# Optimization experiments

Measured on AMD Instinct MI355X. Metric: run time of the kernel, lower is better.

## Reference

```python
import jax, jax.numpy as jnp
import numpy as np

B, F, Q, CHUNK = 2, 8192, 4096, 512
NUM_VERTS = 6000


def _safe_div(n, d):
    return n / jnp.where(d == 0, 1.0, d)


def _bary(a, b, c, p):
    """Barycentric coords of the closest point on triangle (a,b,c) to p.
    All args broadcastable [..., 3]; returns [..., 3] (u, v, w) with
    closest = u*a + v*b + w*c. Ericson, Real-Time Collision Detection."""
    ab = b - a; ac = c - a; ap = p - a
    d1 = jnp.sum(ab * ap, -1); d2 = jnp.sum(ac * ap, -1)
    bp = p - b
    d3 = jnp.sum(ab * bp, -1); d4 = jnp.sum(ac * bp, -1)
    cp_ = p - c
    d5 = jnp.sum(ab * cp_, -1); d6 = jnp.sum(ac * cp_, -1)
    vc = d1 * d4 - d3 * d2
    vb = d5 * d2 - d1 * d6
    va = d3 * d6 - d5 * d4
    v_ab = _safe_div(d1, d1 - d3)
    w_ac = _safe_div(d2, d2 - d6)
    w_bc = _safe_div(d4 - d3, (d4 - d3) + (d5 - d6))
    inv = _safe_div(1.0, va + vb + vc)
    v_in = vb * inv; w_in = vc * inv
    zero = jnp.zeros_like(d1); one = jnp.ones_like(d1)
    conds = [(d1 <= 0) & (d2 <= 0),
             (d3 >= 0) & (d4 <= d3),
             (vc <= 0) & (d1 >= 0) & (d3 <= 0),
             (d6 >= 0) & (d5 <= d6),
             (vb <= 0) & (d2 >= 0) & (d6 <= 0),
             (va <= 0) & (d4 >= d3) & (d5 >= d6)]
    u = jnp.select(conds, [one, zero, 1 - v_ab, zero, 1 - w_ac, zero], 1 - v_in - w_in)
    v = jnp.select(conds, [zero, one, v_ab, zero, zero, 1 - w_bc], v_in)
    w = jnp.select(conds, [zero, zero, zero, one, w_ac, w_bc], w_in)
    return jnp.stack([u, v, w], -1)


def _closest_faces(triangles, points, chunk=CHUNK):
    """Exact closest-triangle index per query point (replaces BVH search).
    triangles [B,F,3,3], points [B,Q,3] -> int32 [B,Q]."""
    tri = jax.lax.stop_gradient(triangles)
    pts = jax.lax.stop_gradient(points)
    bsz, nq = pts.shape[0], pts.shape[1]
    a = tri[:, :, 0]; b = tri[:, :, 1]; c = tri[:, :, 2]  # [B,F,3]

    def one_chunk(p_chunk):  # [B,CH,3]
        pa = p_chunk[:, :, None, :]                       # [B,CH,1,3]
        bc = _bary(a[:, None], b[:, None], c[:, None], pa)  # [B,CH,F,3]
        cp = (bc[..., 0:1] * a[:, None] + bc[..., 1:2] * b[:, None]
              + bc[..., 2:3] * c[:, None])                # [B,CH,F,3]
        d2 = jnp.sum((cp - pa) ** 2, -1)                  # [B,CH,F]
        return jnp.argmin(d2, axis=-1)                    # [B,CH]

    chunks = jnp.moveaxis(pts.reshape(bsz, nq // chunk, chunk, 3), 1, 0)
    idx = jax.lax.map(one_chunk, chunks)                  # [NC,B,CH]
    return jnp.moveaxis(idx, 0, 1).reshape(bsz, nq)


def setup_inputs() -> dict:
    key = jax.random.key(0)
    k1, k2, k3, k4, k5 = jax.random.split(key, 5)
    return {
        'triangles': jax.random.normal(k1, (B, F, 3, 3), dtype=jnp.float32),
        'points': jax.random.normal(k2, (B, Q, 3), dtype=jnp.float32),
        'normals': jax.random.normal(k3, (B, F, 3, 3), dtype=jnp.float32),
        'cmaps': jax.random.normal(k4, (B, F, 3, 3), dtype=jnp.float32),
        'faces': jax.random.randint(k5, (B, F, 3), 0, NUM_VERTS, dtype=jnp.int32),
    }


def reference(triangles, points, normals, cmaps, faces):
    closest_faces = _closest_faces(triangles, points)     # [B,Q]
    idx = closest_faces[:, :, None, None]
    tri_g = jnp.take_along_axis(triangles, idx, axis=1)   # [B,Q,3,3]
    nrm_g = jnp.take_along_axis(normals, idx, axis=1)
    cmp_g = jnp.take_along_axis(cmaps, idx, axis=1)
    bcs = _bary(tri_g[:, :, 0], tri_g[:, :, 1], tri_g[:, :, 2], points)  # [B,Q,3]
    bcs = jnp.clip(bcs, 0.0, 1.0)
    closest_points = jnp.einsum('bqk,bqkd->bqd', bcs, tri_g)
    closest_normals = jnp.einsum('bqk,bqkd->bqd', bcs, nrm_g)
    closest_cmaps = jnp.einsum('bqk,bqkd->bqd', bcs, cmp_g)
    residual = closest_points - points
    closest_fids = jnp.take_along_axis(faces, closest_faces[:, :, None], axis=1)  # [B,Q,3]
    closest_idx = jnp.take_along_axis(
        closest_fids, jnp.argmax(bcs, -1)[:, :, None], axis=2)[..., 0]            # [B,Q]
    return residual, closest_normals, closest_cmaps, closest_idx
```

## Files before the change

kernel.cpp:

```cpp
#include <hip/hip_runtime.h>
#include <float.h>

#define B_   2
#define F_   8192
#define Q_   4096
#define NC   128
#define FC   (F_/NC)
#define PTS  256
#define PPT  4

typedef float f4u __attribute__((ext_vector_type(4), aligned(4)));
typedef unsigned int uint;

__device__ __forceinline__ float clamp01s(float x) {
    return fminf(fmaxf(x, 0.f), 1.f);
}

__device__ __forceinline__ void bary_uvw(
    float ax, float ay, float az,
    float bx, float by, float bz,
    float cx, float cy, float cz,
    float px, float py, float pz,
    float& u, float& v, float& w)
{
#pragma clang fp contract(off)
    float abx = bx - ax, aby = by - ay, abz = bz - az;
    float acx = cx - ax, acy = cy - ay, acz = cz - az;
    float apx = px - ax, apy = py - ay, apz = pz - az;
    float d1 = abx*apx + aby*apy + abz*apz;
    float d2 = acx*apx + acy*apy + acz*apz;
    float bpx = px - bx, bpy = py - by, bpz = pz - bz;
    float d3 = abx*bpx + aby*bpy + abz*bpz;
    float d4 = acx*bpx + acy*bpy + acz*bpz;
    float qx = px - cx, qy = py - cy, qz = pz - cz;
    float d5 = abx*qx + aby*qy + abz*qz;
    float d6 = acx*qx + acy*qy + acz*qz;
    float vc = d1*d4 - d3*d2;
    float vb = d5*d2 - d1*d6;
    float va = d3*d6 - d5*d4;

    bool c1 = (d1 <= 0.f) && (d2 <= 0.f);
    bool c2 = (d3 >= 0.f) && (d4 <= d3);
    bool c3 = (vc <= 0.f) && (d1 >= 0.f) && (d3 <= 0.f);
    bool c4 = (d6 >= 0.f) && (d5 <= d6);
    bool c5 = (vb <= 0.f) && (d2 >= 0.f) && (d6 <= 0.f);
    bool c6 = (va <= 0.f) && (d4 >= d3) && (d5 >= d6);

    bool e1 = c1;
    bool p1 = !c1;
    bool e2 = p1 && c2;
    bool p2 = p1 && !c2;
    bool e3 = p2 && c3;
    bool p3 = p2 && !c3;
    bool e4 = p3 && c4;
    bool p4 = p3 && !c4;
    bool e5 = p4 && c5;
    bool p5 = p4 && !c5;
    bool e6 = p5 && c6;

    float d43 = d4 - d3;
    float d56 = d5 - d6;
    float n  = e3 ? d1        : (e5 ? d2        : (e6 ? d43         : 1.f));
    float dd = e3 ? (d1 - d3) : (e5 ? (d2 - d6) : (e6 ? (d43 + d56) : (va + vb + vc)));
    dd = (dd == 0.f) ? 1.f : dd;
    float t = n / dd;

    float vi = vb * t;
    float wi = vc * t;
    u = e1 ? 1.f : (e2 ? 0.f : (e3 ? 1.f - t : (e4 ? 0.f : (e5 ? 1.f - t : (e6 ? 0.f     : 1.f - vi - wi)))));
    v = e1 ? 0.f : (e2 ? 1.f : (e3 ? t       : (e4 ? 0.f : (e5 ? 0.f     : (e6 ? 1.f - t : vi)))));
    w = e1 ? 0.f : (e2 ? 0.f : (e3 ? 0.f     : (e4 ? 1.f : (e5 ? t       : (e6 ? t       : wi)))));
}

__global__ __launch_bounds__(PTS, 4) void scan_kernel(
    const float* __restrict__ tri, const float* __restrict__ pts,
    uint2* __restrict__ keys)
{
    constexpr int IM = ~(FC - 1);
    __shared__ float4 SC[FC * 5];
    __shared__ float4 SR[FC * 3];
    const int tid = threadIdx.x;
    const int pb = blockIdx.x, cb = blockIdx.y, bb = blockIdx.z;

    if (tid < FC) {
        const float* g = tri + ((size_t)bb * F_ + (size_t)cb * FC + tid) * 9;
        float ax = g[0], ay = g[1], az = g[2];
        float bx = g[3], by = g[4], bz = g[5];
        float cx = g[6], cy = g[7], cz = g[8];
        float abx = bx - ax, aby = by - ay, abz = bz - az;
        float acx = cx - ax, acy = cy - ay, acz = cz - az;
        float daa = abx*abx + aby*aby + abz*abz;
        float dcc = acx*acx + acy*acy + acz*acz;
        float dac = abx*acx + aby*acy + abz*acz;
        float dbc = daa + dcc - 2.f*dac;
        float nn  = daa*dcc - dac*dac;
        SC[tid*5 + 0] = make_float4(abx, aby, abz, -(abx*ax + aby*ay + abz*az));
        SC[tid*5 + 1] = make_float4(acx, acy, acz, -(acx*ax + acy*ay + acz*az));
        SC[tid*5 + 2] = make_float4(-2.f*ax, -2.f*ay, -2.f*az, ax*ax + ay*ay + az*az);
        SC[tid*5 + 3] = make_float4(daa, dcc, dac, nn);
        SC[tid*5 + 4] = make_float4(1.f/daa, 1.f/dcc, 1.f/dbc, 1.f/nn);
        SR[tid*3 + 0] = make_float4(ax, ay, az, 0.f);
        SR[tid*3 + 1] = make_float4(bx, by, bz, 0.f);
        SR[tid*3 + 2] = make_float4(cx, cy, cz, 0.f);
    }
    __syncthreads();

    const int q0 = pb * (PTS * PPT) + tid * PPT;
    const float* p0 = pts + ((size_t)bb * Q_ + q0) * 3;
    f4u l0 = *(const f4u*)(p0);
    f4u l1 = *(const f4u*)(p0 + 4);
    f4u l2 = *(const f4u*)(p0 + 8);
    float pxs[4] = {l0.x, l0.w, l1.z, l2.y};
    float pys[4] = {l0.y, l1.x, l1.w, l2.z};
    float pzs[4] = {l0.z, l1.y, l2.x, l2.w};
    float pps[4];
    #pragma unroll
    for (int p = 0; p < 4; ++p)
        pps[p] = pxs[p]*pxs[p] + pys[p]*pys[p] + pzs[p]*pzs[p];

    int K0[4] = {0x7FFFFFFF, 0x7FFFFFFF, 0x7FFFFFFF, 0x7FFFFFFF};
    int K1[4] = {0x7FFFFFFF, 0x7FFFFFFF, 0x7FFFFFFF, 0x7FFFFFFF};

    #pragma unroll 2
    for (int fl = 0; fl < FC; ++fl) {
        float4 c0 = SC[fl*5 + 0];
        float4 c1 = SC[fl*5 + 1];
        float4 c2 = SC[fl*5 + 2];
        float4 c3 = SC[fl*5 + 3];
        float4 c4 = SC[fl*5 + 4];
        float daa = c3.x, dcc = c3.y, dac = c3.z, nn = c3.w;
        float kk  = daa - dac;
        float dbc = daa + dcc - 2.f*dac;

        #pragma unroll
        for (int p = 0; p < 4; ++p) {
            float px = pxs[p], py = pys[p], pz = pzs[p];
            float d1 = fmaf(c0.x, px, fmaf(c0.y, py, fmaf(c0.z, pz, c0.w)));
            float d2 = fmaf(c1.x, px, fmaf(c1.y, py, fmaf(c1.z, pz, c1.w)));
            float s  = fmaf(c2.x, px, fmaf(c2.y, py, fmaf(c2.z, pz, c2.w)));
            float app = s + pps[p];

            float t1 = d1*dcc - d2*dac;
            float t2 = d2*daa - d1*dac;
            float ts = t1 + t2;
            float t12n = nn - ts;
            float ins  = fminf(fminf(t1, t2), t12n);
            float sgr  = (d1*t1 + d2*t2) * c4.w;

            float td1 = d1 + d1;
            float tab = clamp01s(d1 * c4.x);
            float rab = tab * (td1 - tab*daa);
            float td2 = d2 + d2;
            float tac = clamp01s(d2 * c4.y);
            float rac = tac * (td2 - tac*dcc);
            float d43 = (d2 - d1) + kk;
            float sbc = clamp01s(d43 * c4.z);
            float rbc = (td1 - daa) + sbc * ((d43 + d43) - sbc*dbc);
            float rmax = fmaxf(fmaxf(rab, rac), rbc);

            float red = (ins >= 0.f) ? sgr : rmax;
            float d = app - red;

            int k = (__float_as_int(d) & IM) | fl;
            int m = max(K0[p], k);
            K0[p] = min(K0[p], k);
            K1[p] = min(K1[p], m);
        }
    }

    #pragma unroll
    for (int p = 0; p < 4; ++p) {
        float px = pxs[p], py = pys[p], pz = pzs[p];
        float dbest = FLT_MAX; int fbest = 0x7FFFFFFF;
        #pragma unroll
        for (int j = 0; j < 2; ++j) {
            int lf = (j == 0 ? K0[p] : K1[p]) & (FC - 1);
            float4 ra = SR[lf*3 + 0];
            float4 rb = SR[lf*3 + 1];
            float4 rc = SR[lf*3 + 2];
            float u, v, w;
            bary_uvw(ra.x, ra.y, ra.z, rb.x, rb.y, rb.z, rc.x, rc.y, rc.z,
                     px, py, pz, u, v, w);
            float d2v;
            {
#pragma clang fp contract(off)
                float cpx = u*ra.x + v*rb.x + w*rc.x;
                float cpy = u*ra.y + v*rb.y + w*rc.y;
                float cpz = u*ra.z + v*rb.z + w*rc.z;
                float dx = cpx - px, dy = cpy - py, dz = cpz - pz;
                d2v = dx*dx + dy*dy + dz*dz;
            }
            int face = cb * FC + lf;
            if (d2v < dbest || (d2v == dbest && face < fbest)) { dbest = d2v; fbest = face; }
        }
        keys[((size_t)bb * Q_ + q0 + p) * NC + cb] = make_uint2(__float_as_uint(dbest), (uint)fbest);
    }
}

__global__ __launch_bounds__(256) void finalize_kernel(
    const float* __restrict__ tri, const float* __restrict__ pts,
    const float* __restrict__ nrm, const float* __restrict__ cmp,
    const int* __restrict__ faces,
    const uint2* __restrict__ keys,
    float* __restrict__ out)
{
#pragma clang fp contract(off)
    const int lane = threadIdx.x & 63;
    const int t = blockIdx.x * 4 + (threadIdx.x >> 6);
    const int bb = t >> 12;

    uint4 K = ((const uint4*)keys)[(size_t)t * (NC/2) + lane];
    float dbest = __uint_as_float(K.x); int fbest = (int)K.y;
    float d1v   = __uint_as_float(K.z); int f1v   = (int)K.w;
    if (d1v < dbest || (d1v == dbest && f1v < fbest)) { dbest = d1v; fbest = f1v; }
    for (int off = 32; off > 0; off >>= 1) {
        float od = __shfl_down(dbest, off);
        int   of = __shfl_down(fbest, off);
        if (od < dbest || (od == dbest && of < fbest)) { dbest = od; fbest = of; }
    }
    if (lane != 0) return;

    const float* pp = pts + (size_t)t * 3;
    float px = pp[0], py = pp[1], pz = pp[2];

    const int bestf = fbest;
    const float* tg = tri + ((size_t)bb * F_ + bestf) * 9;
    const float* ng = nrm + ((size_t)bb * F_ + bestf) * 9;
    const float* cg = cmp + ((size_t)bb * F_ + bestf) * 9;
    f4u TA = *(const f4u*)(tg), TB = *(const f4u*)(tg + 4);
    float TC = tg[8];
    f4u NA = *(const f4u*)(ng), NB = *(const f4u*)(ng + 4);
    float NCs = ng[8];
    f4u CA = *(const f4u*)(cg), CB = *(const f4u*)(cg + 4);
    float CC = cg[8];

    float u, v, w;
    bary_uvw(TA.x, TA.y, TA.z, TA.w, TB.x, TB.y, TB.z, TB.w, TC,
             px, py, pz, u, v, w);
    u = fminf(fmaxf(u, 0.f), 1.f);
    v = fminf(fmaxf(v, 0.f), 1.f);
    w = fminf(fmaxf(w, 0.f), 1.f);

    float cpx = u * TA.x + v * TA.w + w * TB.z;
    float cpy = u * TA.y + v * TB.x + w * TB.w;
    float cpz = u * TA.z + v * TB.y + w * TC;
    float nx  = u * NA.x + v * NA.w + w * NB.z;
    float ny  = u * NA.y + v * NB.x + w * NB.w;
    float nz  = u * NA.z + v * NB.y + w * NCs;
    float mx  = u * CA.x + v * CA.w + w * CB.z;
    float my  = u * CA.y + v * CB.x + w * CB.w;
    float mz  = u * CA.z + v * CB.y + w * CC;

    const size_t S3 = (size_t)B_ * Q_ * 3;
    out[(size_t)t * 3 + 0] = cpx - px;
    out[(size_t)t * 3 + 1] = cpy - py;
    out[(size_t)t * 3 + 2] = cpz - pz;
    out[S3 + (size_t)t * 3 + 0] = nx;
    out[S3 + (size_t)t * 3 + 1] = ny;
    out[S3 + (size_t)t * 3 + 2] = nz;
    out[2 * S3 + (size_t)t * 3 + 0] = mx;
    out[2 * S3 + (size_t)t * 3 + 1] = my;
    out[2 * S3 + (size_t)t * 3 + 2] = mz;

    int k = 0; float mm = u;
    if (v > mm) { mm = v; k = 1; }
    if (w > mm) { k = 2; }
    out[3 * S3 + t] = (float)faces[((size_t)bb * F_ + bestf) * 3 + k];
}

extern "C" void kernel_launch(void* const* d_in, const int* in_sizes, int n_in,
                              void* d_out, int out_size, void* d_ws, size_t ws_size,
                              hipStream_t stream) {
    const float* tri   = (const float*)d_in[0];
    const float* pts   = (const float*)d_in[1];
    const float* nrm   = (const float*)d_in[2];
    const float* cmp   = (const float*)d_in[3];
    const int*   faces = (const int*)d_in[4];
    float* out = (float*)d_out;

    uint2* keys = (uint2*)d_ws;

    dim3 g1(Q_ / (PTS * PPT), NC, B_);
    scan_kernel<<<g1, PTS, 0, stream>>>(tri, pts, keys);
    finalize_kernel<<<(B_ * Q_) / 4, 256, 0, stream>>>(
        tri, pts, nrm, cmp, faces, keys, out);
}
```

Baseline: 146.3 us.

## Precompute triangle constants in separate kernel and read them from global memory

Moves the per-triangle constant setup out of the scan kernel into a new precompute kernel that writes six float4s per face to workspace. The scan kernel then drops its shared-memory staging and barrier and reads the constants straight from global memory, which are uniform across the block and so likely become scalar loads. Points per thread drop from four to two and the occupancy hint rises from 4 to 8. This trades one extra launch and fewer points per constant fetch for no LDS use and higher occupancy.

```diff
diff --git a/kernel.cpp b/kernel.cpp
--- a/kernel.cpp
+++ b/kernel.cpp
@@ -7,9 +7,10 @@
 #define NC   128
 #define FC   (F_/NC)
 #define PTS  256
-#define PPT  4
+#define PPT  2
 
 typedef float f4u __attribute__((ext_vector_type(4), aligned(4)));
+typedef float f2u __attribute__((ext_vector_type(2), aligned(8)));
 typedef unsigned int uint;
 
 __device__ __forceinline__ float clamp01s(float x) {
@@ -72,121 +73,145 @@
     w = e1 ? 0.f : (e2 ? 0.f : (e3 ? 0.f     : (e4 ? 1.f : (e5 ? t       : (e6 ? t       : wi)))));
 }
 
-__global__ __launch_bounds__(PTS, 4) void scan_kernel(
+__global__ void precompute_kernel(const float* __restrict__ tri,
+                                  float4* __restrict__ cons)
+{
+    int i = blockIdx.x * blockDim.x + threadIdx.x;
+    if (i >= B_ * F_) return;
+    const float* g = tri + (size_t)i * 9;
+    float ax = g[0], ay = g[1], az = g[2];
+    float bx = g[3], by = g[4], bz = g[5];
+    float cx = g[6], cy = g[7], cz = g[8];
+    float abx = bx - ax, aby = by - ay, abz = bz - az;
+    float acx = cx - ax, acy = cy - ay, acz = cz - az;
+    float daa = abx*abx + aby*aby + abz*abz;
+    float dcc = acx*acx + acy*acy + acz*acz;
+    float dac = abx*acx + aby*acy + abz*acz;
+    float dbc = daa + dcc - 2.f*dac;
+    float nn  = daa*dcc - dac*dac;
+    float4* o = cons + (size_t)i * 6;
+    o[0] = make_float4(abx, aby, abz, -(abx*ax + aby*ay + abz*az));
+    o[1] = make_float4(acx, acy, acz, -(acx*ax + acy*ay + acz*az));
+    o[2] = make_float4(-2.f*ax, -2.f*ay, -2.f*az, ax*ax + ay*ay + az*az);
+    o[3] = make_float4(daa, dcc, -dac, nn);
+    o[4] = make_float4(1.f/daa, 1.f/dcc, 1.f/dbc, 1.f/nn);
+    o[5] = make_float4(daa - dac, dbc, 0.f, 0.f);
+}
+
+__global__ __launch_bounds__(PTS, 8) void scan_kernel(
     const float* __restrict__ tri, const float* __restrict__ pts,
-    uint2* __restrict__ keys)
+    const float4* __restrict__ cons, uint2* __restrict__ keys)
 {
     constexpr int IM = ~(FC - 1);
-    __shared__ float4 SC[FC * 5];
-    __shared__ float4 SR[FC * 3];
     const int tid = threadIdx.x;
     const int pb = blockIdx.x, cb = blockIdx.y, bb = blockIdx.z;
 
-    if (tid < FC) {
-        const float* g = tri + ((size_t)bb * F_ + (size_t)cb * FC + tid) * 9;
-        float ax = g[0], ay = g[1], az = g[2];
-        float bx = g[3], by = g[4], bz = g[5];
-        float cx = g[6], cy = g[7], cz = g[8];
-        float abx = bx - ax, aby = by - ay, abz = bz - az;
-        float acx = cx - ax, acy = cy - ay, acz = cz - az;
-        float daa = abx*abx + aby*aby + abz*abz;
-        float dcc = acx*acx + acy*acy + acz*acz;
-        float dac = abx*acx + aby*acy + abz*acz;
-        float dbc = daa + dcc - 2.f*dac;
-        float nn  = daa*dcc - dac*dac;
-        SC[tid*5 + 0] = make_float4(abx, aby, abz, -(abx*ax + aby*ay + abz*az));
-        SC[tid*5 + 1] = make_float4(acx, acy, acz, -(acx*ax + acy*ay + acz*az));
-        SC[tid*5 + 2] = make_float4(-2.f*ax, -2.f*ay, -2.f*az, ax*ax + ay*ay + az*az);
-        SC[tid*5 + 3] = make_float4(daa, dcc, dac, nn);
-        SC[tid*5 + 4] = make_float4(1.f/daa, 1.f/dcc, 1.f/dbc, 1.f/nn);
-        SR[tid*3 + 0] = make_float4(ax, ay, az, 0.f);
-        SR[tid*3 + 1] = make_float4(bx, by, bz, 0.f);
-        SR[tid*3 + 2] = make_float4(cx, cy, cz, 0.f);
-    }
-    __syncthreads();
-
     const int q0 = pb * (PTS * PPT) + tid * PPT;
     const float* p0 = pts + ((size_t)bb * Q_ + q0) * 3;
-    f4u l0 = *(const f4u*)(p0);
-    f4u l1 = *(const f4u*)(p0 + 4);
-    f4u l2 = *(const f4u*)(p0 + 8);
-    float pxs[4] = {l0.x, l0.w, l1.z, l2.y};
-    float pys[4] = {l0.y, l1.x, l1.w, l2.z};
-    float pzs[4] = {l0.z, l1.y, l2.x, l2.w};
-    float pps[4];
-    #pragma unroll
-    for (int p = 0; p < 4; ++p)
-        pps[p] = pxs[p]*pxs[p] + pys[p]*pys[p] + pzs[p]*pzs[p];
-
-    int K0[4] = {0x7FFFFFFF, 0x7FFFFFFF, 0x7FFFFFFF, 0x7FFFFFFF};
-    int K1[4] = {0x7FFFFFFF, 0x7FFFFFFF, 0x7FFFFFFF, 0x7FFFFFFF};
+    f2u m0 = *(const f2u*)(p0);
+    f2u m1 = *(const f2u*)(p0 + 2);
+    f2u m2 = *(const f2u*)(p0 + 4);
+    float px0 = m0.x, py0 = m0.y, pz0 = m1.x;
+    float px1 = m1.y, py1 = m2.x, pz1 = m2.y;
+    float pp0 = px0*px0 + py0*py0 + pz0*pz0;
+    float pp1 = px1*px1 + py1*py1 + pz1*pz1;
+
+    const float4* ct = cons + ((size_t)bb * F_ + (size_t)cb * FC) * 6;
+
+    int K00 = 0x7FFFFFFF, K01 = 0x7FFFFFFF;
+    int K10 = 0x7FFFFFFF, K11 = 0x7FFFFFFF;
 
     #pragma unroll 2
     for (int fl = 0; fl < FC; ++fl) {
-        float4 c0 = SC[fl*5 + 0];
-        float4 c1 = SC[fl*5 + 1];
-        float4 c2 = SC[fl*5 + 2];
-        float4 c3 = SC[fl*5 + 3];
-        float4 c4 = SC[fl*5 + 4];
-        float daa = c3.x, dcc = c3.y, dac = c3.z, nn = c3.w;
-        float kk  = daa - dac;
-        float dbc = daa + dcc - 2.f*dac;
-
-        #pragma unroll
-        for (int p = 0; p < 4; ++p) {
-            float px = pxs[p], py = pys[p], pz = pzs[p];
-            float d1 = fmaf(c0.x, px, fmaf(c0.y, py, fmaf(c0.z, pz, c0.w)));
-            float d2 = fmaf(c1.x, px, fmaf(c1.y, py, fmaf(c1.z, pz, c1.w)));
-            float s  = fmaf(c2.x, px, fmaf(c2.y, py, fmaf(c2.z, pz, c2.w)));
-            float app = s + pps[p];
-
-            float t1 = d1*dcc - d2*dac;
-            float t2 = d2*daa - d1*dac;
-            float ts = t1 + t2;
-            float t12n = nn - ts;
+        float4 T0 = ct[fl*6 + 0];
+        float4 T1 = ct[fl*6 + 1];
+        float4 T2 = ct[fl*6 + 2];
+        float4 T3 = ct[fl*6 + 3];
+        float4 T4 = ct[fl*6 + 4];
+        float4 T5 = ct[fl*6 + 5];
+
+        {
+            float d1 = fmaf(T0.x, px0, fmaf(T0.y, py0, fmaf(T0.z, pz0, T0.w)));
+            float d2 = fmaf(T1.x, px0, fmaf(T1.y, py0, fmaf(T1.z, pz0, T1.w)));
+            float s  = fmaf(T2.x, px0, fmaf(T2.y, py0, fmaf(T2.z, pz0, T2.w)));
+            float app = s + pp0;
+            float t1 = fmaf(d2, T3.z, d1 * T3.y);
+            float t2 = fmaf(d1, T3.z, d2 * T3.x);
+            float t12n = T3.w - (t1 + t2);
             float ins  = fminf(fminf(t1, t2), t12n);
-            float sgr  = (d1*t1 + d2*t2) * c4.w;
-
+            float sgr  = fmaf(d2, t2, d1 * t1) * T4.w;
             float td1 = d1 + d1;
-            float tab = clamp01s(d1 * c4.x);
-            float rab = tab * (td1 - tab*daa);
+            float tab = clamp01s(d1 * T4.x);
+            float rab = tab * fmaf(-tab, T3.x, td1);
             float td2 = d2 + d2;
-            float tac = clamp01s(d2 * c4.y);
-            float rac = tac * (td2 - tac*dcc);
-            float d43 = (d2 - d1) + kk;
-            float sbc = clamp01s(d43 * c4.z);
-            float rbc = (td1 - daa) + sbc * ((d43 + d43) - sbc*dbc);
+            float tac = clamp01s(d2 * T4.y);
+            float rac = tac * fmaf(-tac, T3.y, td2);
+            float d43 = (d2 - d1) + T5.x;
+            float sbc = clamp01s(d43 * T4.z);
+            float rbc = (td1 - T3.x) + sbc * fmaf(-sbc, T5.y, d43 + d43);
             float rmax = fmaxf(fmaxf(rab, rac), rbc);
-
             float red = (ins >= 0.f) ? sgr : rmax;
-            float d = app - red;
-
-            int k = (__float_as_int(d) & IM) | fl;
-            int m = max(K0[p], k);
-            K0[p] = min(K0[p], k);
-            K1[p] = min(K1[p], m);
+            float dd = app - red;
+            int k = (__float_as_int(dd) & IM) | fl;
+            int m = max(K00, k);
+            K00 = min(K00, k);
+            K01 = min(K01, m);
+        }
+        {
+            float d1 = fmaf(T0.x, px1, fmaf(T0.y, py1, fmaf(T0.z, pz1, T0.w)));
+            float d2 = fmaf(T1.x, px1, fmaf(T1.y, py1, fmaf(T1.z, pz1, T1.w)));
+            float s  = fmaf(T2.x, px1, fmaf(T2.y, py1, fmaf(T2.z, pz1, T2.w)));
+            float app = s + pp1;
+            float t1 = fmaf(d2, T3.z, d1 * T3.y);
+            float t2 = fmaf(d1, T3.z, d2 * T3.x);
+            float t12n = T3.w - (t1 + t2);
+            float ins  = fminf(fminf(t1, t2), t12n);
+            float sgr  = fmaf(d2, t2, d1 * t1) * T4.w;
+            float td1 = d1 + d1;
+            float tab = clamp01s(d1 * T4.x);
+            float rab = tab * fmaf(-tab, T3.x, td1);
+            float td2 = d2 + d2;
+            float tac = clamp01s(d2 * T4.y);
+            float rac = tac * fmaf(-tac, T3.y, td2);
+            float d43 = (d2 - d1) + T5.x;
+            float sbc = clamp01s(d43 * T4.z);
+            float rbc = (td1 - T3.x) + sbc * fmaf(-sbc, T5.y, d43 + d43);
+            float rmax = fmaxf(fmaxf(rab, rac), rbc);
+            float red = (ins >= 0.f) ? sgr : rmax;
+            float dd = app - red;
+            int k = (__float_as_int(dd) & IM) | fl;
+            int m = max(K10, k);
+            K10 = min(K10, k);
+            K11 = min(K11, m);
         }
     }
 
+    float pxs[2] = {px0, px1};
+    float pys[2] = {py0, py1};
+    float pzs[2] = {pz0, pz1};
+    int kk0[2] = {K00, K10};
+    int kk1[2] = {K01, K11};
+
     #pragma unroll
-    for (int p = 0; p < 4; ++p) {
+    for (int p = 0; p < 2; ++p) {
         float px = pxs[p], py = pys[p], pz = pzs[p];
         float dbest = FLT_MAX; int fbest = 0x7FFFFFFF;
         #pragma unroll
         for (int j = 0; j < 2; ++j) {
-            int lf = (j == 0 ? K0[p] : K1[p]) & (FC - 1);
-            float4 ra = SR[lf*3 + 0];
-            float4 rb = SR[lf*3 + 1];
-            float4 rc = SR[lf*3 + 2];
+            int lf = (j == 0 ? kk0[p] : kk1[p]) & (FC - 1);
+            const float* tg = tri + ((size_t)bb * F_ + (size_t)cb * FC + lf) * 9;
+            f4u ra4 = *(const f4u*)(tg);
+            f4u rb4 = *(const f4u*)(tg + 4);
+            float rc8 = tg[8];
             float u, v, w;
-            bary_uvw(ra.x, ra.y, ra.z, rb.x, rb.y, rb.z, rc.x, rc.y, rc.z,
-                     px, py, pz, u, v, w);
+            bary_uvw(ra4.x, ra4.y, ra4.z, ra4.w, rb4.x, rb4.y,
+                     rb4.z, rb4.w, rc8, px, py, pz, u, v, w);
             float d2v;
             {
 #pragma clang fp contract(off)
-                float cpx = u*ra.x + v*rb.x + w*rc.x;
-                float cpy = u*ra.y + v*rb.y + w*rc.y;
-                float cpz = u*ra.z + v*rb.z + w*rc.z;
+                float cpx = u*ra4.x + v*ra4.w + w*rb4.z;
+                float cpy = u*ra4.y + v*rb4.x + w*rb4.w;
+                float cpz = u*ra4.z + v*rb4.y + w*rc8;
                 float dx = cpx - px, dy = cpy - py, dz = cpz - pz;
                 d2v = dx*dx + dy*dy + dz*dz;
             }
@@ -278,10 +303,13 @@
     const int*   faces = (const int*)d_in[4];
     float* out = (float*)d_out;
 
-    uint2* keys = (uint2*)d_ws;
+    uint2*  keys = (uint2*)d_ws;
+    float4* cons = (float4*)((char*)d_ws + (size_t)B_ * Q_ * NC * sizeof(uint2));
+
+    precompute_kernel<<<(B_ * F_ + 255) / 256, 256, 0, stream>>>(tri, cons);
 
     dim3 g1(Q_ / (PTS * PPT), NC, B_);
-    scan_kernel<<<g1, PTS, 0, stream>>>(tri, pts, keys);
+    scan_kernel<<<g1, PTS, 0, stream>>>(tri, pts, cons, keys);
     finalize_kernel<<<(B_ * Q_) / 4, 256, 0, stream>>>(
         tri, pts, nrm, cmp, faces, keys, out);
 }
```

New measurement: 145.7 us. About the same (-0.4%).
